# Kernel tuning notes

Hardware: AMD Instinct MI355X
Metric: run time of the kernel (lower is better)

The kernel has to match this reference:

```python
import jax, jax.numpy as jnp
import numpy as np


def setup_inputs() -> dict:
    key = jax.random.key(0)
    kx, kq, kk, kv = jax.random.split(key, 4)
    B, S, D_IN, H, D_OUT = 2, 2048, 768, 12, 64
    scale = 0.02
    return {
        "x": jax.random.normal(kx, (B, S, D_IN), dtype=jnp.float32),
        "Wq": jax.random.normal(kq, (H, D_IN, D_OUT), dtype=jnp.float32) * scale,
        "Wk": jax.random.normal(kk, (H, D_IN, D_OUT), dtype=jnp.float32) * scale,
        "Wv": jax.random.normal(kv, (H, D_IN, D_OUT), dtype=jnp.float32) * scale,
    }


def reference(x, Wq, Wk, Wv):
    # x: [B, S, d_in]; Wq/Wk/Wv: [H, d_in, d_out] (stacked per-head Linear weights, no bias)
    B, S, _ = x.shape
    H, _, d_out = Wq.shape
    q = jnp.einsum("bsd,hde->bhse", x, Wq)  # [B, H, S, d_out]
    k = jnp.einsum("bsd,hde->bhse", x, Wk)
    v = jnp.einsum("bsd,hde->bhse", x, Wv)
    scores = jnp.einsum("bhse,bhte->bhst", q, k) / jnp.sqrt(jnp.float32(d_out))
    causal = jnp.tril(jnp.ones((S, S), dtype=bool))  # True = keep
    scores = jnp.where(causal, scores, jnp.float32(-jnp.inf))
    attn = jax.nn.softmax(scores, axis=-1)  # dropout = 0.0 -> identity
    ctx = jnp.einsum("bhst,bhte->bhse", attn, v)  # [B, H, S, d_out]
    # concat heads along last dim: [B, S, H*d_out]
    return ctx.transpose(0, 2, 1, 3).reshape(B, S, H * d_out)
```

## Files before the change

kernel.cpp:

```cpp
#include <hip/hip_runtime.h>
#include <hip/hip_bf16.h>


typedef short bf16x8 __attribute__((ext_vector_type(8)));
typedef short bf16x4 __attribute__((ext_vector_type(4)));
typedef float f32x4  __attribute__((ext_vector_type(4)));

#define MFMA16(a, b, c)  __builtin_amdgcn_mfma_f32_16x16x32_bf16((a), (b), (c), 0, 0, 0)
#define MFMAK16(a, b, c) __builtin_amdgcn_mfma_f32_16x16x16bf16_1k((a), (b), (c), 0, 0, 0)

static __device__ __forceinline__ unsigned short f2bf(float f) {
    unsigned int u = __builtin_bit_cast(unsigned int, f);
    u += 0x7fffu + ((u >> 16) & 1u);
    return (unsigned short)(u >> 16);
}

static __device__ __forceinline__ int sw(int row, int cb) {
    return (row << 7) + (cb ^ ((row & 7) << 4));
}

static __device__ __forceinline__ void gld16(const void* g, void* l) {
    __builtin_amdgcn_global_load_lds(
        (__attribute__((address_space(1))) void*)g,
        (__attribute__((address_space(3))) void*)l, 16, 0, 0);
}

__global__ __launch_bounds__(256) void prep(const float* __restrict__ x,
                                            const float* __restrict__ Wq,
                                            const float* __restrict__ Wk,
                                            const float* __restrict__ Wv,
                                            char* __restrict__ xb,
                                            char* __restrict__ wtb) {
    __shared__ float tile[64][65];
    const int bid = blockIdx.x;
    const int t = threadIdx.x;
    if (bid < 768) {
        const int stile = bid & 63, ks = bid >> 6;
        const int row = t >> 2, k16 = (t & 3) * 16;
        const float* src = x + (size_t)(stile * 64 + row) * 768 + ks * 64 + k16;
        char* img = xb + ((size_t)stile * 12 + ks) * 8192;
        const float4 v0 = *(const float4*)(src);
        const float4 v1 = *(const float4*)(src + 4);
        const float4 v2 = *(const float4*)(src + 8);
        const float4 v3 = *(const float4*)(src + 12);
        bf16x8 o0, o1;
        o0[0] = (short)f2bf(v0.x); o0[1] = (short)f2bf(v0.y);
        o0[2] = (short)f2bf(v0.z); o0[3] = (short)f2bf(v0.w);
        o0[4] = (short)f2bf(v1.x); o0[5] = (short)f2bf(v1.y);
        o0[6] = (short)f2bf(v1.z); o0[7] = (short)f2bf(v1.w);
        o1[0] = (short)f2bf(v2.x); o1[1] = (short)f2bf(v2.y);
        o1[2] = (short)f2bf(v2.z); o1[3] = (short)f2bf(v2.w);
        o1[4] = (short)f2bf(v3.x); o1[5] = (short)f2bf(v3.y);
        o1[6] = (short)f2bf(v3.z); o1[7] = (short)f2bf(v3.w);
        *(bf16x8*)(img + sw(row, k16 * 2)) = o0;
        *(bf16x8*)(img + sw(row, k16 * 2 + 16)) = o1;
    } else {
        const int idx = bid - 768;
        const int wh = idx % 36, dt = idx / 36;
        const int w = wh / 12, h = wh % 12;
        const float* W = (w == 0) ? Wq : (w == 1) ? Wk : Wv;
        for (int i = 0; i < 4; ++i) {
            int c = t + i * 256;
            int d = c >> 4, e4 = (c & 15) * 4;
            const float4 v = *(const float4*)(W + (size_t)(h * 768 + dt * 64 + d) * 64 + e4);
            tile[d][e4 + 0] = v.x; tile[d][e4 + 1] = v.y;
            tile[d][e4 + 2] = v.z; tile[d][e4 + 3] = v.w;
        }
        __syncthreads();
        char* img = wtb + ((size_t)(wh * 12) + dt) * 8192;
        for (int i = 0; i < 4; ++i) {
            int c = t + i * 256;
            int e = c >> 4, d4 = (c & 15) * 4;
            ushort4 o;
            o.x = f2bf(tile[d4 + 0][e]); o.y = f2bf(tile[d4 + 1][e]);
            o.z = f2bf(tile[d4 + 2][e]); o.w = f2bf(tile[d4 + 3][e]);
            *(ushort4*)(img + e * 128 + ((d4 * 2) ^ ((e & 7) << 4))) = o;
        }
    }
}

__global__ __launch_bounds__(256) void proj_qkv(const char* __restrict__ xb,
                                                const char* __restrict__ wtb,
                                                unsigned short* __restrict__ q,
                                                unsigned short* __restrict__ ksw,
                                                char* __restrict__ vsw) {
    __shared__ __align__(16) char smem[65536];
    const int stile = blockIdx.x;
    const int h = blockIdx.y;
    const int t = threadIdx.x;
    const int wave = t >> 6, lane = t & 63;
    const int lhi = lane >> 4, llo = lane & 15;
    const int wr = wave >> 1, wc = wave & 1;

    const char* asrc = xb + (size_t)stile * 12 * 8192;

    f32x4 acc[3][2][2] = {};

    #define STAGE(KS, BUF)                                                       \
        do {                                                                     \
            const char* s0 = asrc + (KS) * 8192;                                 \
            char* d0 = smem + (BUF) * 32768;                                     \
            gld16(s0 + t * 16, d0 + t * 16);                                     \
            gld16(s0 + t * 16 + 4096, d0 + t * 16 + 4096);                       \
            for (int w3 = 0; w3 < 3; ++w3) {                                     \
                const char* s1 = wtb + ((size_t)((w3 * 12 + h) * 12) + (KS)) * 8192; \
                char* d1 = smem + (BUF) * 32768 + (1 + w3) * 8192;               \
                gld16(s1 + t * 16, d1 + t * 16);                                 \
                gld16(s1 + t * 16 + 4096, d1 + t * 16 + 4096);                   \
            }                                                                    \
        } while (0)

    STAGE(0, 0);
    __syncthreads();
    int cur = 0;
    for (int ks = 0; ks < 12; ++ks) {
        if (ks < 11) STAGE(ks + 1, cur ^ 1);
        char* Alds = smem + cur * 32768;
        #pragma unroll
        for (int kk = 0; kk < 2; ++kk) {
            bf16x8 a[2];
            #pragma unroll
            for (int m = 0; m < 2; ++m)
                a[m] = *(const bf16x8*)(Alds + sw(wr * 32 + m * 16 + llo, kk * 64 + lhi * 16));
            #pragma unroll
            for (int w3 = 0; w3 < 3; ++w3) {
                char* Blds = Alds + (1 + w3) * 8192;
                #pragma unroll
                for (int n = 0; n < 2; ++n) {
                    bf16x8 b = *(const bf16x8*)(Blds + sw(wc * 32 + n * 16 + llo, kk * 64 + lhi * 16));
                    #pragma unroll
                    for (int m = 0; m < 2; ++m)
                        acc[w3][m][n] = MFMA16(a[m], b, acc[w3][m][n]);
                }
            }
        }
        __syncthreads();
        cur ^= 1;
    }
    #undef STAGE

    const float SCALE_Q = 0.18033688011112042f;
    const int bglob = stile >> 5, ktile = stile & 31;
    const int bh = bglob * 12 + h;
    #pragma unroll
    for (int m = 0; m < 2; ++m)
        for (int n = 0; n < 2; ++n)
            for (int r = 0; r < 4; ++r) {
                int s = (stile * 64 + wr * 32 + m * 16 + lhi * 4 + r) & 2047;
                int e = wc * 32 + n * 16 + llo;
                q[(size_t)(bh * 2048 + s) * 64 + e] = f2bf(acc[0][m][n][r] * SCALE_Q);
            }
    unsigned short* kdst = ksw + ((size_t)bh * 32 + ktile) * 4096;
    #pragma unroll
    for (int m = 0; m < 2; ++m)
        for (int n = 0; n < 2; ++n)
            for (int r = 0; r < 4; ++r) {
                int kk = wr * 32 + m * 16 + lhi * 4 + r;
                int e = wc * 32 + n * 16 + llo;
                kdst[kk * 64 + (e ^ ((kk & 7) << 3))] = f2bf(acc[1][m][n][r]);
            }
    char* vtimg = smem;
    __syncthreads();
    #pragma unroll
    for (int m = 0; m < 2; ++m)
        for (int n = 0; n < 2; ++n)
            for (int r = 0; r < 4; ++r) {
                int kk = wr * 32 + m * 16 + lhi * 4 + r;
                int e = wc * 32 + n * 16 + llo;
                int pos = (((kk >> 2) & 3) * 32 + (kk >> 4) * 8 + (kk & 3) * 2) ^ ((e & 7) << 4);
                *(unsigned short*)(vtimg + e * 128 + pos) = f2bf(acc[2][m][n][r]);
            }
    __syncthreads();
    {
        char* dst = vsw + ((size_t)bh * 32 + ktile) * 8192;
        #pragma unroll
        for (int i = 0; i < 2; ++i)
            *(float4*)(dst + t * 16 + i * 4096) =
                *(const float4*)(vtimg + t * 16 + i * 4096);
    }
}

__global__ __launch_bounds__(256) void attn(const unsigned short* __restrict__ Q,
                                            const char* __restrict__ Ksw,
                                            const char* __restrict__ Vsw,
                                            float* __restrict__ out,
                                            float* __restrict__ Obuf,
                                            float* __restrict__ mlbuf) {
    __shared__ __align__(16) char smem[32768];
    const int t = threadIdx.x, wave = t >> 6, lane = t & 63;
    const int lhi = lane >> 4, llo = lane & 15;
    const int round = blockIdx.x >> 8, pos = blockIdx.x & 255;
    const int rank = (round & 1) ? (round << 8) + (255 - pos) : (int)blockIdx.x;
    int bh, qt, kts, kte;
    bool split; int part = 0;
    if (rank < 432) {
        bh = rank % 24;
        const int j = rank / 24;
        if (j < 16)      { qt = 16 + j; part = 0; kts = 0;  kte = 15; split = true;  }
        else if (j == 16){ qt = 15;              kts = 0;  kte = 15; split = false; }
        else             { qt = 31;     part = 1; kts = 16; kte = 31; split = true;  }
    } else {
        const int g = (rank - 432) / 48;
        const int r2 = (rank - 432) % 48;
        bh = r2 % 24;
        const int s = 15 - g;
        if (r2 / 24 == 0) { qt = s - 1;            kts = 0;  kte = qt; split = false; }
        else              { qt = s + 15; part = 1; kts = 16; kte = qt; split = true;  }
    }
    const unsigned short* Qg = Q + (size_t)bh * 2048 * 64;
    const char* Kg = Ksw + (size_t)bh * 32 * 8192;
    const char* Vg = Vsw + (size_t)bh * 32 * 8192;

    const int q0 = qt * 64 + wave * 16;
    bf16x8 qa[2];
    #pragma unroll
    for (int kk = 0; kk < 2; ++kk)
        qa[kk] = *(const bf16x8*)(Qg + (size_t)(q0 + llo) * 64 + kk * 32 + lhi * 8);

    f32x4 acc[4] = {};
    float m_r = -1e30f, l_r = 0.f;

    #define ASTAGE(KT, BUF)                                              \
        do {                                                             \
            const char* ks_ = Kg + (size_t)(KT) * 8192;                  \
            const char* vs_ = Vg + (size_t)(KT) * 8192;                  \
            char* kd = smem + (BUF) * 8192;                              \
            char* vd = smem + 16384 + (BUF) * 8192;                      \
            gld16(ks_ + t * 16, kd + t * 16);                            \
            gld16(ks_ + t * 16 + 4096, kd + t * 16 + 4096);              \
            gld16(vs_ + t * 16, vd + t * 16);                            \
            gld16(vs_ + t * 16 + 4096, vd + t * 16 + 4096);              \
        } while (0)

    ASTAGE(kts, 0);
    __syncthreads();
    int cur = 0;
    for (int kt = kts; kt <= kte; ++kt) {
        if (kt < kte) ASTAGE(kt + 1, cur ^ 1);
        char* Kb = smem + cur * 8192;
        char* Vb = smem + 16384 + cur * 8192;

        f32x4 sc[4];
        __builtin_amdgcn_s_setprio(1);
        #pragma unroll
        for (int n = 0; n < 4; ++n) {
            f32x4 z = {};
            #pragma unroll
            for (int kk = 0; kk < 2; ++kk) {
                bf16x8 bk = *(const bf16x8*)(Kb + sw(n * 16 + llo, kk * 64 + lhi * 16));
                z = MFMA16(bk, qa[kk], z);
            }
            sc[n] = z;
        }
        __builtin_amdgcn_s_setprio(0);
        bf16x8 vfr[4][2];
        #pragma unroll
        for (int n = 0; n < 4; ++n) {
            const int row = n * 16 + llo;
            vfr[n][0] = *(const bf16x8*)(Vb + sw(row, lhi * 32));
            vfr[n][1] = *(const bf16x8*)(Vb + sw(row, lhi * 32 + 16));
        }
        if (kt == qt) {
            #pragma unroll
            for (int n = 0; n < 4; ++n)
                #pragma unroll
                for (int r = 0; r < 4; ++r)
                    if (kt * 64 + n * 16 + lhi * 4 + r > q0 + llo) sc[n][r] = -1e30f;
        }
        float pmax = fmaxf(
            fmaxf(fmaxf(fmaxf(sc[0][0], sc[0][1]), fmaxf(sc[0][2], sc[0][3])),
                  fmaxf(fmaxf(sc[1][0], sc[1][1]), fmaxf(sc[1][2], sc[1][3]))),
            fmaxf(fmaxf(fmaxf(sc[2][0], sc[2][1]), fmaxf(sc[2][2], sc[2][3])),
                  fmaxf(fmaxf(sc[3][0], sc[3][1]), fmaxf(sc[3][2], sc[3][3]))));
        if (__any(pmax > m_r + 8.0f)) {
            float tm = fmaxf(pmax, __shfl_xor(pmax, 16, 64));
            tm = fmaxf(tm, __shfl_xor(tm, 32, 64));
            float nm = fmaxf(m_r, tm);
            float corr = exp2f(m_r - nm);
            m_r = nm;
            l_r *= corr;
            #pragma unroll
            for (int n = 0; n < 4; ++n)
                #pragma unroll
                for (int r = 0; r < 4; ++r) acc[n][r] *= corr;
        }
        bf16x4 pf[4];
        float ps = 0.f;
        #pragma unroll
        for (int kb = 0; kb < 4; ++kb) {
            float p0 = exp2f(sc[kb][0] - m_r), p1 = exp2f(sc[kb][1] - m_r);
            float p2 = exp2f(sc[kb][2] - m_r), p3 = exp2f(sc[kb][3] - m_r);
            ps += (p0 + p1) + (p2 + p3);
            unsigned int w0, w1;
            asm("v_cvt_pk_bf16_f32 %0, %1, %2" : "=v"(w0) : "v"(p0), "v"(p1));
            asm("v_cvt_pk_bf16_f32 %0, %1, %2" : "=v"(w1) : "v"(p2), "v"(p3));
            unsigned long long u = ((unsigned long long)w1 << 32) | w0;
            pf[kb] = __builtin_bit_cast(bf16x4, u);
        }
        l_r += ps;
        __builtin_amdgcn_s_setprio(1);
        #pragma unroll
        for (int n = 0; n < 4; ++n) {
            f32x4 a = acc[n];
            a = MFMAK16(__builtin_shufflevector(vfr[n][0], vfr[n][0], 0, 1, 2, 3), pf[0], a);
            a = MFMAK16(__builtin_shufflevector(vfr[n][0], vfr[n][0], 4, 5, 6, 7), pf[1], a);
            a = MFMAK16(__builtin_shufflevector(vfr[n][1], vfr[n][1], 0, 1, 2, 3), pf[2], a);
            a = MFMAK16(__builtin_shufflevector(vfr[n][1], vfr[n][1], 4, 5, 6, 7), pf[3], a);
            acc[n] = a;
        }
        __builtin_amdgcn_s_setprio(0);
        if (kt < kte) __syncthreads();
        cur ^= 1;
    }
    #undef ASTAGE
    l_r += __shfl_xor(l_r, 16, 64);
    l_r += __shfl_xor(l_r, 32, 64);
    if (split) {
        const int p = ((bh * 16) + (qt - 16)) * 2 + part;
        float* Ob = Obuf + (size_t)p * 4096;
        const int qrow = wave * 16 + llo;
        #pragma unroll
        for (int n = 0; n < 4; ++n) {
            float4 o;
            o.x = acc[n][0]; o.y = acc[n][1]; o.z = acc[n][2]; o.w = acc[n][3];
            *(float4*)(Ob + qrow * 64 + n * 16 + lhi * 4) = o;
        }
        if (lhi == 0) {
            float2 ml; ml.x = m_r; ml.y = l_r;
            *(float2*)(mlbuf + (size_t)p * 128 + qrow * 2) = ml;
        }
    } else {
        const float inv = 1.0f / l_r;
        const int b = bh / 12, h = bh - b * 12;
        #pragma unroll
        for (int n = 0; n < 4; ++n) {
            float4 o;
            o.x = acc[n][0] * inv; o.y = acc[n][1] * inv;
            o.z = acc[n][2] * inv; o.w = acc[n][3] * inv;
            *(float4*)(out + (size_t)(b * 2048 + q0 + llo) * 768 + h * 64 + n * 16 + lhi * 4) = o;
        }
    }
}

__global__ __launch_bounds__(256) void combine(const float* __restrict__ Obuf,
                                               const float* __restrict__ mlbuf,
                                               float* __restrict__ out) {
    const int bid = blockIdx.x;
    const int bh = bid % 24, qt = 16 + bid / 24;
    const int b = bh / 12, h = bh - b * 12;
    const int t = threadIdx.x;
    const int r = t >> 2, c0 = (t & 3) * 16;
    const int p0 = ((bh * 16) + (qt - 16)) * 2;
    const float2 ml0 = *(const float2*)(mlbuf + (size_t)p0 * 128 + r * 2);
    const float2 ml1 = *(const float2*)(mlbuf + (size_t)(p0 + 1) * 128 + r * 2);
    const float mm = fmaxf(ml0.x, ml1.x);
    const float w0 = exp2f(ml0.x - mm), w1 = exp2f(ml1.x - mm);
    const float inv = 1.0f / (ml0.y * w0 + ml1.y * w1);
    const float* s0 = Obuf + (size_t)p0 * 4096 + r * 64 + c0;
    const float* s1 = s0 + 4096;
    float* dst = out + (size_t)(b * 2048 + qt * 64 + r) * 768 + h * 64 + c0;
    #pragma unroll
    for (int i = 0; i < 4; ++i) {
        const float4 a = *(const float4*)(s0 + i * 4);
        const float4 c = *(const float4*)(s1 + i * 4);
        float4 o;
        o.x = (a.x * w0 + c.x * w1) * inv;
        o.y = (a.y * w0 + c.y * w1) * inv;
        o.z = (a.z * w0 + c.z * w1) * inv;
        o.w = (a.w * w0 + c.w * w1) * inv;
        *(float4*)(dst + i * 4) = o;
    }
}

extern "C" void kernel_launch(void* const* d_in, const int* in_sizes, int n_in,
                              void* d_out, int out_size, void* d_ws, size_t ws_size,
                              hipStream_t stream) {
    const float* x  = (const float*)d_in[0];
    const float* Wq = (const float*)d_in[1];
    const float* Wk = (const float*)d_in[2];
    const float* Wv = (const float*)d_in[3];
    float* out = (float*)d_out;

    char* ws = (char*)d_ws;
    char*           wtb   = ws;
    unsigned short* q     = (unsigned short*)(ws + 3538944);
    unsigned short* ksw   = (unsigned short*)(ws + 9830400);
    char*           vsw   = (char*)(ws + 16121856);
    char*           xb    = (char*)(ws + 22413312);
    float*          Obuf  = (float*)(ws + 28704768);
    float*          mlbuf = (float*)(ws + 41287680);

    hipLaunchKernelGGL(prep, dim3(1200), dim3(256), 0, stream, x, Wq, Wk, Wv, xb, wtb);
    hipLaunchKernelGGL(proj_qkv, dim3(64, 12), dim3(256), 0, stream,
                       xb, wtb, q, ksw, vsw);
    hipLaunchKernelGGL(attn, dim3(1152), dim3(256), 0, stream,
                       q, (const char*)ksw, vsw, out, Obuf, mlbuf);
    hipLaunchKernelGGL(combine, dim3(384), dim3(256), 0, stream, Obuf, mlbuf, out);
}
```

Baseline: 68.33 us.

## Software-pipeline QK^T one tile ahead of softmax and PV in attention loop

Restructures the attention main loop so the QK^T scores for the next K tile are computed before the softmax and PV of the current tile. The goal is to overlap MFMA work with the exp/softmax VALU work and to issue the next-next tile's loads later. This adds an extra barrier per iteration and another set of score registers, which can raise register pressure and lower occupancy.

```diff
diff --git a/kernel.cpp b/kernel.cpp
--- a/kernel.cpp
+++ b/kernel.cpp
@@ -232,46 +232,49 @@
             gld16(vs_ + t * 16 + 4096, vd + t * 16 + 4096);              \
         } while (0)
 
+    #define QKT(SC, KB)                                                          \
+        do {                                                                     \
+            __builtin_amdgcn_s_setprio(1);                                       \
+            _Pragma("unroll")                                                    \
+            for (int n = 0; n < 4; ++n) {                                        \
+                f32x4 z = {};                                                    \
+                _Pragma("unroll")                                                \
+                for (int kk = 0; kk < 2; ++kk) {                                 \
+                    bf16x8 bk = *(const bf16x8*)((KB) + sw(n * 16 + llo,         \
+                                                           kk * 64 + lhi * 16)); \
+                    z = MFMA16(bk, qa[kk], z);                                   \
+                }                                                                \
+                (SC)[n] = z;                                                     \
+            }                                                                    \
+            __builtin_amdgcn_s_setprio(0);                                       \
+        } while (0)
+
     ASTAGE(kts, 0);
     __syncthreads();
-    int cur = 0;
+    f32x4 scA[4];
+    QKT(scA, smem);
+    if (kts < kte) ASTAGE(kts + 1, 1);
+
+    int curV = 0;
     for (int kt = kts; kt <= kte; ++kt) {
-        if (kt < kte) ASTAGE(kt + 1, cur ^ 1);
-        char* Kb = smem + cur * 8192;
-        char* Vb = smem + 16384 + cur * 8192;
-
-        f32x4 sc[4];
-        __builtin_amdgcn_s_setprio(1);
-        #pragma unroll
-        for (int n = 0; n < 4; ++n) {
-            f32x4 z = {};
-            #pragma unroll
-            for (int kk = 0; kk < 2; ++kk) {
-                bf16x8 bk = *(const bf16x8*)(Kb + sw(n * 16 + llo, kk * 64 + lhi * 16));
-                z = MFMA16(bk, qa[kk], z);
-            }
-            sc[n] = z;
-        }
-        __builtin_amdgcn_s_setprio(0);
-        bf16x8 vfr[4][2];
-        #pragma unroll
-        for (int n = 0; n < 4; ++n) {
-            const int row = n * 16 + llo;
-            vfr[n][0] = *(const bf16x8*)(Vb + sw(row, lhi * 32));
-            vfr[n][1] = *(const bf16x8*)(Vb + sw(row, lhi * 32 + 16));
+        const bool haveNext = (kt < kte);
+        f32x4 scB[4];
+        if (haveNext) {
+            __syncthreads();
+            QKT(scB, smem + (curV ^ 1) * 8192);
         }
         if (kt == qt) {
             #pragma unroll
             for (int n = 0; n < 4; ++n)
                 #pragma unroll
                 for (int r = 0; r < 4; ++r)
-                    if (kt * 64 + n * 16 + lhi * 4 + r > q0 + llo) sc[n][r] = -1e30f;
+                    if (kt * 64 + n * 16 + lhi * 4 + r > q0 + llo) scA[n][r] = -1e30f;
         }
         float pmax = fmaxf(
-            fmaxf(fmaxf(fmaxf(sc[0][0], sc[0][1]), fmaxf(sc[0][2], sc[0][3])),
-                  fmaxf(fmaxf(sc[1][0], sc[1][1]), fmaxf(sc[1][2], sc[1][3]))),
-            fmaxf(fmaxf(fmaxf(sc[2][0], sc[2][1]), fmaxf(sc[2][2], sc[2][3])),
-                  fmaxf(fmaxf(sc[3][0], sc[3][1]), fmaxf(sc[3][2], sc[3][3]))));
+            fmaxf(fmaxf(fmaxf(scA[0][0], scA[0][1]), fmaxf(scA[0][2], scA[0][3])),
+                  fmaxf(fmaxf(scA[1][0], scA[1][1]), fmaxf(scA[1][2], scA[1][3]))),
+            fmaxf(fmaxf(fmaxf(scA[2][0], scA[2][1]), fmaxf(scA[2][2], scA[2][3])),
+                  fmaxf(fmaxf(scA[3][0], scA[3][1]), fmaxf(scA[3][2], scA[3][3]))));
         if (__any(pmax > m_r + 8.0f)) {
             float tm = fmaxf(pmax, __shfl_xor(pmax, 16, 64));
             tm = fmaxf(tm, __shfl_xor(tm, 32, 64));
@@ -288,8 +291,8 @@
         float ps = 0.f;
         #pragma unroll
         for (int kb = 0; kb < 4; ++kb) {
-            float p0 = exp2f(sc[kb][0] - m_r), p1 = exp2f(sc[kb][1] - m_r);
-            float p2 = exp2f(sc[kb][2] - m_r), p3 = exp2f(sc[kb][3] - m_r);
+            float p0 = exp2f(scA[kb][0] - m_r), p1 = exp2f(scA[kb][1] - m_r);
+            float p2 = exp2f(scA[kb][2] - m_r), p3 = exp2f(scA[kb][3] - m_r);
             ps += (p0 + p1) + (p2 + p3);
             unsigned int w0, w1;
             asm("v_cvt_pk_bf16_f32 %0, %1, %2" : "=v"(w0) : "v"(p0), "v"(p1));
@@ -298,20 +301,34 @@
             pf[kb] = __builtin_bit_cast(bf16x4, u);
         }
         l_r += ps;
-        __builtin_amdgcn_s_setprio(1);
-        #pragma unroll
-        for (int n = 0; n < 4; ++n) {
-            f32x4 a = acc[n];
-            a = MFMAK16(__builtin_shufflevector(vfr[n][0], vfr[n][0], 0, 1, 2, 3), pf[0], a);
-            a = MFMAK16(__builtin_shufflevector(vfr[n][0], vfr[n][0], 4, 5, 6, 7), pf[1], a);
-            a = MFMAK16(__builtin_shufflevector(vfr[n][1], vfr[n][1], 0, 1, 2, 3), pf[2], a);
-            a = MFMAK16(__builtin_shufflevector(vfr[n][1], vfr[n][1], 4, 5, 6, 7), pf[3], a);
-            acc[n] = a;
-        }
-        __builtin_amdgcn_s_setprio(0);
-        if (kt < kte) __syncthreads();
-        cur ^= 1;
-    }
+        {
+            char* Vb = smem + 16384 + curV * 8192;
+            __builtin_amdgcn_s_setprio(1);
+            #pragma unroll
+            for (int n = 0; n < 4; ++n) {
+                const int row = n * 16 + llo;
+                bf16x8 v8a = *(const bf16x8*)(Vb + sw(row, lhi * 32));
+                bf16x8 v8b = *(const bf16x8*)(Vb + sw(row, lhi * 32 + 16));
+                f32x4 a = acc[n];
+                a = MFMAK16(__builtin_shufflevector(v8a, v8a, 0, 1, 2, 3), pf[0], a);
+                a = MFMAK16(__builtin_shufflevector(v8a, v8a, 4, 5, 6, 7), pf[1], a);
+                a = MFMAK16(__builtin_shufflevector(v8b, v8b, 0, 1, 2, 3), pf[2], a);
+                a = MFMAK16(__builtin_shufflevector(v8b, v8b, 4, 5, 6, 7), pf[3], a);
+                acc[n] = a;
+            }
+            __builtin_amdgcn_s_setprio(0);
+        }
+        if (kt + 1 < kte) {
+            __syncthreads();
+            ASTAGE(kt + 2, curV);
+        }
+        if (haveNext) {
+            #pragma unroll
+            for (int n = 0; n < 4; ++n) scA[n] = scB[n];
+        }
+        curV ^= 1;
+    }
+    #undef QKT
     #undef ASTAGE
     l_r += __shfl_xor(l_r, 16, 64);
     l_r += __shfl_xor(l_r, 32, 64);
```

Measured after the change: 74.26 us. 1.09x slower.
